# Kernel optimization log

Measured on AMD Instinct MI355X. Metric: run time of the kernel, lower is better.

Reference implementation:

```python
import jax, jax.numpy as jnp
import numpy as np

B, D, R = 4096, 1024, 256
DT = 0.01
DT_SCALE = 1.0

# Yoshida 4th-order coefficients
_W1 = 1.0 / (2.0 - 2.0 ** (1.0 / 3.0))
_W0 = -(2.0 ** (1.0 / 3.0)) / (2.0 - 2.0 ** (1.0 / 3.0))
C1 = _W1 / 2.0
C2 = (_W0 + _W1) / 2.0
C3 = C2
C4 = C1
D1 = _W1
D2 = _W0
D3 = _W1


def setup_inputs() -> dict:
    key = jax.random.key(0)
    k1, k2, k3, k4, k5 = jax.random.split(key, 5)
    x = jax.random.normal(k1, (B, D), dtype=jnp.float32)
    v = jax.random.normal(k2, (B, D), dtype=jnp.float32)
    force = jax.random.normal(k3, (B, D), dtype=jnp.float32)
    # low-rank christoffel factors, scaled for numerical stability
    U = jax.random.normal(k4, (R, D), dtype=jnp.float32) * (1.0 / np.sqrt(D))
    W = jax.random.normal(k5, (D, R), dtype=jnp.float32) * (1.0 / np.sqrt(R))
    return {"x": x, "v": v, "force": force, "U": U, "W": W}


def _christoffel(tv, tx, U, W):
    # Gamma(v) = W @ (U v)^2  (low-rank quadratic form; x unused, matching
    # the gfn yoshida_fused(U, W) signature)
    h = jnp.einsum("rd,bd->br", U, tv)  # [B, R]
    return jnp.einsum("dr,br->bd", W, h * h)  # [B, D]


def reference(x, v, force, U, W):
    dt = DT * DT_SCALE

    def acceleration(tx, tv):
        return -_christoffel(tv, tx, U, W) + force

    x1 = x + C1 * dt * v
    v1 = v + D1 * dt * acceleration(x1, v)
    x2 = x1 + C2 * dt * v1
    v2 = v1 + D2 * dt * acceleration(x2, v1)
    x3 = x2 + C3 * dt * v2
    v3 = v2 + D3 * dt * acceleration(x3, v2)
    x_final = x3 + C4 * dt * v3
    return (x_final, v3)
```

## Files before the change

### kernel.cpp

```cpp
#include <hip/hip_runtime.h>


#define BSZ 4096
#define DD 1024
#define RR 256
#define NCOPY 4
#define COPY_BYTES (512u * 1024u)

typedef unsigned char uchar;
typedef long long i64;
typedef __attribute__((ext_vector_type(2))) long i64x2;
typedef __attribute__((ext_vector_type(4))) float f32x4;
typedef __attribute__((ext_vector_type(4))) unsigned int uint4v;

__device__ inline unsigned int f2q4(float a, float b, float c, float d) {
    int lo = __builtin_amdgcn_cvt_pk_fp8_f32(a, b, 0, false);
    int hi = __builtin_amdgcn_cvt_pk_fp8_f32(c, d, lo, true);
    return (unsigned int)hi;
}
__device__ inline uchar f2q1(float x) {
    return (uchar)(__builtin_amdgcn_cvt_pk_fp8_f32(x, x, 0, false) & 0xff);
}

__global__ __launch_bounds__(256) void pack_uw_kernel(
    const float* __restrict__ U, const float* __restrict__ W,
    uchar* __restrict__ ws)
{
    const int g = blockIdx.x * 256 + threadIdx.x;
    const float* src;
    size_t off;
    float sc;
    if (g < 16384) {
        const int l = g & 63, p = (g >> 6) & 15, nt = g >> 10;
        src = U + (size_t)(nt * 16 + (l & 15)) * DD + p * 64 + (l >> 4) * 8;
        off = ((size_t)nt << 14) + (p << 10) + (l << 4);
        sc = 8.0f;
    } else {
        const int g2 = g - 16384;
        const int l = g2 & 63, p = (g2 >> 6) & 3, dt_ = g2 >> 8;
        src = W + (size_t)(dt_ * 16 + (l & 15)) * RR + p * 64 + (l >> 4) * 8;
        off = (size_t)(256 * 1024) + ((size_t)dt_ << 12) + (p << 10) + (l << 4);
        sc = 16.0f;
    }
    const float4 x0 = *reinterpret_cast<const float4*>(src);
    const float4 x1 = *reinterpret_cast<const float4*>(src + 4);
    const float4 y0 = *reinterpret_cast<const float4*>(src + 32);
    const float4 y1 = *reinterpret_cast<const float4*>(src + 36);
    uint4v o;
    o.x = f2q4(sc * x0.x, sc * x0.y, sc * x0.z, sc * x0.w);
    o.y = f2q4(sc * x1.x, sc * x1.y, sc * x1.z, sc * x1.w);
    o.z = f2q4(sc * y0.x, sc * y0.y, sc * y0.z, sc * y0.w);
    o.w = f2q4(sc * y1.x, sc * y1.y, sc * y1.z, sc * y1.w);
    #pragma unroll
    for (int c = 0; c < NCOPY; ++c)
        *reinterpret_cast<uint4v*>(ws + (size_t)c * COPY_BYTES + off) = o;
}

__global__ __launch_bounds__(1024) void yoshida_fused_kernel(
    const float* __restrict__ x_in,
    const float* __restrict__ v_in,
    const float* __restrict__ force,
    const uchar* __restrict__ ws,
    float* __restrict__ x_out,
    float* __restrict__ v_out)
{
    __shared__ __align__(16) uchar vS[16][1040];
    __shared__ __align__(16) uchar H2S[16][272];

    const int tid = threadIdx.x;
    const int w = tid >> 6, l = tid & 63;
    const int m = l & 15, q = l >> 4;
    const int b0 = blockIdx.x * 16;
    const int d0 = w * 64;

    const uchar* base = ws + (size_t)((blockIdx.x >> 3) & (NCOPY - 1)) * COPY_BYTES;

    constexpr double CBRT2 = 1.2599210498948731647672106072782;
    constexpr double W1c = 1.0 / (2.0 - CBRT2);
    constexpr double W0c = -CBRT2 * W1c;
    constexpr double DTd = 0.01 * 1.0;
    const float dcoef[3] = {(float)(W1c * DTd), (float)(W0c * DTd), (float)(W1c * DTd)};
    const float xcoef[3] = {(float)((W0c + W1c) * 0.5), (float)((W0c + W1c) * 0.5),
                            (float)(W1c * 0.5)};
    const float c1  = (float)(W1c * 0.5);
    const float dtf = (float)DTd;
    const float invdt = (float)(1.0 / DTd);

    float vreg[16], xacc[16], freg[16];
    #pragma unroll
    for (int t = 0; t < 4; ++t)
        #pragma unroll
        for (int i = 0; i < 4; ++i) {
            const size_t gidx = (size_t)(b0 + q * 4 + i) * DD + d0 + t * 16 + m;
            const float vv = v_in[gidx];
            vreg[t * 4 + i] = vv;
            xacc[t * 4 + i] = invdt * x_in[gidx] + c1 * vv;
            freg[t * 4 + i] = force[gidx];
        }

    {
        const int row = tid >> 6;
        const int col = (tid & 63) * 16;
        const float* sp = v_in + (size_t)(b0 + row) * DD + col;
        const float4 f0 = *reinterpret_cast<const float4*>(sp);
        const float4 f1 = *reinterpret_cast<const float4*>(sp + 4);
        const float4 f2 = *reinterpret_cast<const float4*>(sp + 8);
        const float4 f3 = *reinterpret_cast<const float4*>(sp + 12);
        uint4v pk;
        pk.x = f2q4(f0.x, f0.y, f0.z, f0.w);
        pk.y = f2q4(f1.x, f1.y, f1.z, f1.w);
        pk.z = f2q4(f2.x, f2.y, f2.z, f2.w);
        pk.w = f2q4(f3.x, f3.y, f3.z, f3.w);
        *reinterpret_cast<uint4v*>(&vS[row][col]) = pk;
    }

    const uchar* up = base + ((size_t)w << 14) + (l << 4);
    const uchar* wp = base + 256 * 1024 + ((size_t)(w * 4) << 12) + (l << 4);

    #pragma unroll
    for (int s = 0; s < 3; ++s) {
        __syncthreads();

        f32x4 a0 = {0.f, 0.f, 0.f, 0.f}, a1 = {0.f, 0.f, 0.f, 0.f};
        #pragma unroll
        for (int p = 0; p < 16; ++p) {
            const i64x2 bb = *reinterpret_cast<const i64x2*>(up + (p << 10));
            const i64 af0 = *reinterpret_cast<const i64*>(&vS[m][p * 64 + q * 8]);
            const i64 af1 = *reinterpret_cast<const i64*>(&vS[m][p * 64 + 32 + q * 8]);
            a0 = __builtin_amdgcn_mfma_f32_16x16x32_fp8_fp8(af0, bb.x, a0, 0, 0, 0);
            a1 = __builtin_amdgcn_mfma_f32_16x16x32_fp8_fp8(af1, bb.y, a1, 0, 0, 0);
        }
        #pragma unroll
        for (int i = 0; i < 4; ++i) {
            const float h8 = a0[i] + a1[i];
            H2S[q * 4 + i][w * 16 + m] = f2q1(h8 * h8 * 0.015625f);
        }
        __syncthreads();

        f32x4 accB[4];
        #pragma unroll
        for (int t = 0; t < 4; ++t) accB[t] = (f32x4){0.f, 0.f, 0.f, 0.f};
        #pragma unroll
        for (int p = 0; p < 4; ++p) {
            const i64 ha0 = *reinterpret_cast<const i64*>(&H2S[m][p * 64 + q * 8]);
            const i64 ha1 = *reinterpret_cast<const i64*>(&H2S[m][p * 64 + 32 + q * 8]);
            #pragma unroll
            for (int t = 0; t < 4; ++t) {
                const i64x2 wb = *reinterpret_cast<const i64x2*>(wp + (t << 12) + (p << 10));
                accB[t] = __builtin_amdgcn_mfma_f32_16x16x32_fp8_fp8(ha0, wb.x, accB[t], 0, 0, 0);
                accB[t] = __builtin_amdgcn_mfma_f32_16x16x32_fp8_fp8(ha1, wb.y, accB[t], 0, 0, 0);
            }
        }

        const float ddt = dcoef[s], cx = xcoef[s], gsc = dcoef[s] * 0.0625f;
        #pragma unroll
        for (int t = 0; t < 4; ++t)
            #pragma unroll
            for (int i = 0; i < 4; ++i) {
                const float vn = vreg[t * 4 + i] + ddt * freg[t * 4 + i]
                                 - gsc * accB[t][i];
                vreg[t * 4 + i] = vn;
                xacc[t * 4 + i] += cx * vn;
                vS[q * 4 + i][d0 + t * 16 + m] = f2q1(vn);
            }
    }

    #pragma unroll
    for (int t = 0; t < 4; ++t)
        #pragma unroll
        for (int i = 0; i < 4; ++i) {
            const size_t g = (size_t)(b0 + q * 4 + i) * DD + d0 + t * 16 + m;
            x_out[g] = dtf * xacc[t * 4 + i];
            v_out[g] = vreg[t * 4 + i];
        }
}

extern "C" void kernel_launch(void* const* d_in, const int* in_sizes, int n_in,
                              void* d_out, int out_size, void* d_ws, size_t ws_size,
                              hipStream_t stream) {
    const float* x     = (const float*)d_in[0];
    const float* v     = (const float*)d_in[1];
    const float* force = (const float*)d_in[2];
    const float* U     = (const float*)d_in[3];
    const float* W     = (const float*)d_in[4];

    float* x_out = (float*)d_out;
    float* v_out = x_out + (size_t)BSZ * DD;

    uchar* ws = (uchar*)d_ws;

    pack_uw_kernel<<<dim3(128), dim3(256), 0, stream>>>(U, W, ws);
    yoshida_fused_kernel<<<dim3(BSZ / 16), dim3(1024), 0, stream>>>(
        x, v, force, ws, x_out, v_out);
}
```

Measured before the change: 125.9 us.

## Move force and x accumulator to LDS, preload W into registers, double-buffer U

Keeps force in LDS as fp16 and the x accumulator in LDS as fp32, freeing registers, and defers the x_in load to the final stage. W fragments are held in registers across all three stages, U fragments are prefetched in a double buffer, and a minimum-blocks hint is added to launch bounds. The aim is to cut register pressure and hide global load latency. The cost is much more LDS per block (about 115KB), which limits resident blocks, and fp16 rounding of force.

Measured after the change: 138.5 us. +10.0%, slower.

```diff
diff --git a/kernel.cpp b/kernel.cpp
--- a/kernel.cpp
+++ b/kernel.cpp
@@ -12,6 +12,7 @@
 typedef __attribute__((ext_vector_type(2))) long i64x2;
 typedef __attribute__((ext_vector_type(4))) float f32x4;
 typedef __attribute__((ext_vector_type(4))) unsigned int uint4v;
+typedef __attribute__((ext_vector_type(4))) _Float16 f16x4;
 
 __device__ inline unsigned int f2q4(float a, float b, float c, float d) {
     int lo = __builtin_amdgcn_cvt_pk_fp8_f32(a, b, 0, false);
@@ -56,7 +57,7 @@
         *reinterpret_cast<uint4v*>(ws + (size_t)c * COPY_BYTES + off) = o;
 }
 
-__global__ __launch_bounds__(1024) void yoshida_fused_kernel(
+__global__ __launch_bounds__(1024, 4) void yoshida_fused_kernel(
     const float* __restrict__ x_in,
     const float* __restrict__ v_in,
     const float* __restrict__ force,
@@ -66,6 +67,8 @@
 {
     __shared__ __align__(16) uchar vS[16][1040];
     __shared__ __align__(16) uchar H2S[16][272];
+    __shared__ __align__(16) _Float16 fS[16][1032];
+    __shared__ __align__(16) float xaS[16][1028];
 
     const int tid = threadIdx.x;
     const int w = tid >> 6, l = tid & 63;
@@ -84,19 +87,16 @@
                             (float)(W1c * 0.5)};
     const float c1  = (float)(W1c * 0.5);
     const float dtf = (float)DTd;
-    const float invdt = (float)(1.0 / DTd);
-
-    float vreg[16], xacc[16], freg[16];
+
+    const uchar* up = base + ((size_t)w << 14) + (l << 4);
+    const uchar* wp = base + 256 * 1024 + ((size_t)(w * 4) << 12) + (l << 4);
+
+    i64x2 wreg[4][4];
     #pragma unroll
     for (int t = 0; t < 4; ++t)
         #pragma unroll
-        for (int i = 0; i < 4; ++i) {
-            const size_t gidx = (size_t)(b0 + q * 4 + i) * DD + d0 + t * 16 + m;
-            const float vv = v_in[gidx];
-            vreg[t * 4 + i] = vv;
-            xacc[t * 4 + i] = invdt * x_in[gidx] + c1 * vv;
-            freg[t * 4 + i] = force[gidx];
-        }
+        for (int p = 0; p < 4; ++p)
+            wreg[t][p] = *reinterpret_cast<const i64x2*>(wp + (t << 12) + (p << 10));
 
     {
         const int row = tid >> 6;
@@ -114,8 +114,31 @@
         *reinterpret_cast<uint4v*>(&vS[row][col]) = pk;
     }
 
-    const uchar* up = base + ((size_t)w << 14) + (l << 4);
-    const uchar* wp = base + 256 * 1024 + ((size_t)(w * 4) << 12) + (l << 4);
+    {
+        const float* sp = force + (size_t)(b0 + w) * DD;
+        #pragma unroll
+        for (int c = 0; c < 4; ++c) {
+            const float4 f = *reinterpret_cast<const float4*>(sp + l * 4 + c * 256);
+            f16x4 h;
+            h.x = (_Float16)f.x; h.y = (_Float16)f.y;
+            h.z = (_Float16)f.z; h.w = (_Float16)f.w;
+            *reinterpret_cast<f16x4*>(&fS[w][l * 4 + c * 256]) = h;
+        }
+    }
+
+    float vreg[16];
+    #pragma unroll
+    for (int t = 0; t < 4; ++t)
+        #pragma unroll
+        for (int i = 0; i < 4; ++i)
+            vreg[t * 4 + i] =
+                v_in[(size_t)(b0 + q * 4 + i) * DD + d0 + t * 16 + m];
+
+    i64x2 ub[2][2];
+    ub[0][0] = *reinterpret_cast<const i64x2*>(up);
+    ub[0][1] = *reinterpret_cast<const i64x2*>(up + 1024);
+
+    float xreg[16];
 
     #pragma unroll
     for (int s = 0; s < 3; ++s) {
@@ -123,12 +146,26 @@
 
         f32x4 a0 = {0.f, 0.f, 0.f, 0.f}, a1 = {0.f, 0.f, 0.f, 0.f};
         #pragma unroll
-        for (int p = 0; p < 16; ++p) {
-            const i64x2 bb = *reinterpret_cast<const i64x2*>(up + (p << 10));
-            const i64 af0 = *reinterpret_cast<const i64*>(&vS[m][p * 64 + q * 8]);
-            const i64 af1 = *reinterpret_cast<const i64*>(&vS[m][p * 64 + 32 + q * 8]);
-            a0 = __builtin_amdgcn_mfma_f32_16x16x32_fp8_fp8(af0, bb.x, a0, 0, 0, 0);
-            a1 = __builtin_amdgcn_mfma_f32_16x16x32_fp8_fp8(af1, bb.y, a1, 0, 0, 0);
+        for (int pb = 0; pb < 8; ++pb) {
+            if (pb < 7) {
+                ub[(pb + 1) & 1][0] = *reinterpret_cast<const i64x2*>(
+                    up + (((pb + 1) * 2 + 0) << 10));
+                ub[(pb + 1) & 1][1] = *reinterpret_cast<const i64x2*>(
+                    up + (((pb + 1) * 2 + 1) << 10));
+            } else if (s < 2) {
+                ub[0][0] = *reinterpret_cast<const i64x2*>(up);
+                ub[0][1] = *reinterpret_cast<const i64x2*>(up + 1024);
+            }
+            #pragma unroll
+            for (int j = 0; j < 2; ++j) {
+                const int p = pb * 2 + j;
+                const i64 af0 = *reinterpret_cast<const i64*>(&vS[m][p * 64 + q * 8]);
+                const i64 af1 = *reinterpret_cast<const i64*>(&vS[m][p * 64 + 32 + q * 8]);
+                a0 = __builtin_amdgcn_mfma_f32_16x16x32_fp8_fp8(
+                         af0, ub[pb & 1][j].x, a0, 0, 0, 0);
+                a1 = __builtin_amdgcn_mfma_f32_16x16x32_fp8_fp8(
+                         af1, ub[pb & 1][j].y, a1, 0, 0, 0);
+            }
         }
         #pragma unroll
         for (int i = 0; i < 4; ++i) {
@@ -137,6 +174,15 @@
         }
         __syncthreads();
 
+        if (s == 2) {
+            #pragma unroll
+            for (int t = 0; t < 4; ++t)
+                #pragma unroll
+                for (int i = 0; i < 4; ++i)
+                    xreg[t * 4 + i] =
+                        x_in[(size_t)(b0 + q * 4 + i) * DD + d0 + t * 16 + m];
+        }
+
         f32x4 accB[4];
         #pragma unroll
         for (int t = 0; t < 4; ++t) accB[t] = (f32x4){0.f, 0.f, 0.f, 0.f};
@@ -146,9 +192,10 @@
             const i64 ha1 = *reinterpret_cast<const i64*>(&H2S[m][p * 64 + 32 + q * 8]);
             #pragma unroll
             for (int t = 0; t < 4; ++t) {
-                const i64x2 wb = *reinterpret_cast<const i64x2*>(wp + (t << 12) + (p << 10));
-                accB[t] = __builtin_amdgcn_mfma_f32_16x16x32_fp8_fp8(ha0, wb.x, accB[t], 0, 0, 0);
-                accB[t] = __builtin_amdgcn_mfma_f32_16x16x32_fp8_fp8(ha1, wb.y, accB[t], 0, 0, 0);
+                accB[t] = __builtin_amdgcn_mfma_f32_16x16x32_fp8_fp8(
+                              ha0, wreg[t][p].x, accB[t], 0, 0, 0);
+                accB[t] = __builtin_amdgcn_mfma_f32_16x16x32_fp8_fp8(
+                              ha1, wreg[t][p].y, accB[t], 0, 0, 0);
             }
         }
 
@@ -157,22 +204,25 @@
         for (int t = 0; t < 4; ++t)
             #pragma unroll
             for (int i = 0; i < 4; ++i) {
-                const float vn = vreg[t * 4 + i] + ddt * freg[t * 4 + i]
-                                 - gsc * accB[t][i];
+                const int r = q * 4 + i, c = d0 + t * 16 + m;
+                const float ff = (float)fS[r][c];
+                const float vold = vreg[t * 4 + i];
+                const float vn = vold + ddt * ff - gsc * accB[t][i];
                 vreg[t * 4 + i] = vn;
-                xacc[t * 4 + i] += cx * vn;
-                vS[q * 4 + i][d0 + t * 16 + m] = f2q1(vn);
-            }
-    }
-
-    #pragma unroll
-    for (int t = 0; t < 4; ++t)
-        #pragma unroll
-        for (int i = 0; i < 4; ++i) {
-            const size_t g = (size_t)(b0 + q * 4 + i) * DD + d0 + t * 16 + m;
-            x_out[g] = dtf * xacc[t * 4 + i];
-            v_out[g] = vreg[t * 4 + i];
-        }
+                if (s == 0) {
+                    xaS[r][c] = c1 * vold + cx * vn;
+                    vS[r][c] = f2q1(vn);
+                } else if (s == 1) {
+                    xaS[r][c] += cx * vn;
+                    vS[r][c] = f2q1(vn);
+                } else {
+                    const float xa = xaS[r][c] + cx * vn;
+                    const size_t g = (size_t)(b0 + r) * DD + c;
+                    x_out[g] = xreg[t * 4 + i] + dtf * xa;
+                    v_out[g] = vn;
+                }
+            }
+    }
 }
 
 extern "C" void kernel_launch(void* const* d_in, const int* in_sizes, int n_in,
```

## Recast Yoshida steps in rank space using precomputed U·W and bf16 MFMA

Applied to the files above, without the earlier changes.

Rewrites the integrator algebraically so the three stages run in the rank-256 space. It precomputes M = U·W with a new atomic-add kernel and tracks h = U·v, updating it through g = U·force and M·h². The per-stage D×R W GEMMs are replaced by one final W projection that gives both the v and x corrections (P and Q coefficient sums). Precision moves from fp8 to bf16 MFMA, which roughly doubles the operand bytes per FLOP. A third launch is added, along with an atomicAdd reduction and large LDS use (152KB per block), which limits occupancy to one block per CU.

Result: slower. 148.5 us (+18.0%).

```diff
diff --git a/kernel.cpp b/kernel.cpp
--- a/kernel.cpp
+++ b/kernel.cpp
@@ -4,56 +4,85 @@
 #define BSZ 4096
 #define DD 1024
 #define RR 256
-#define NCOPY 4
-#define COPY_BYTES (512u * 1024u)
+
+#define U_OFF 0u
+#define W_OFF (512u * 1024u)
+#define M_OFF (1024u * 1024u)
 
 typedef unsigned char uchar;
 typedef long long i64;
-typedef __attribute__((ext_vector_type(2))) long i64x2;
+typedef unsigned int uint;
 typedef __attribute__((ext_vector_type(4))) float f32x4;
-typedef __attribute__((ext_vector_type(4))) unsigned int uint4v;
-
-__device__ inline unsigned int f2q4(float a, float b, float c, float d) {
-    int lo = __builtin_amdgcn_cvt_pk_fp8_f32(a, b, 0, false);
-    int hi = __builtin_amdgcn_cvt_pk_fp8_f32(c, d, lo, true);
-    return (unsigned int)hi;
-}
-__device__ inline uchar f2q1(float x) {
-    return (uchar)(__builtin_amdgcn_cvt_pk_fp8_f32(x, x, 0, false) & 0xff);
-}
-
-__global__ __launch_bounds__(256) void pack_uw_kernel(
+typedef __attribute__((ext_vector_type(4))) uint uint4v;
+typedef __attribute__((ext_vector_type(8))) short short8;
+
+__device__ inline uint f2bf1(float x) {
+    uint u = __builtin_bit_cast(uint, x);
+    return (u + 0x7FFFu + ((u >> 16) & 1u)) >> 16;
+}
+__device__ inline uint f2bf2(float lo, float hi) {
+    return f2bf1(lo) | (f2bf1(hi) << 16);
+}
+
+__global__ __launch_bounds__(256) void pack_kernel(
     const float* __restrict__ U, const float* __restrict__ W,
     uchar* __restrict__ ws)
 {
     const int g = blockIdx.x * 256 + threadIdx.x;
+    *reinterpret_cast<float*>(ws + M_OFF + (size_t)g * 4) = 0.0f;
+
+    const int l = g & 63;
     const float* src;
-    size_t off;
-    float sc;
-    if (g < 16384) {
-        const int l = g & 63, p = (g >> 6) & 15, nt = g >> 10;
-        src = U + (size_t)(nt * 16 + (l & 15)) * DD + p * 64 + (l >> 4) * 8;
-        off = ((size_t)nt << 14) + (p << 10) + (l << 4);
-        sc = 8.0f;
+    size_t dst;
+    if (g < 32768) {
+        const int slice = g >> 6, nt = slice >> 5, p = slice & 31;
+        src = U + (size_t)(nt * 16 + (l & 15)) * DD + p * 32 + (l >> 4) * 8;
+        dst = U_OFF + (size_t)slice * 1024 + l * 16;
     } else {
-        const int g2 = g - 16384;
-        const int l = g2 & 63, p = (g2 >> 6) & 3, dt_ = g2 >> 8;
-        src = W + (size_t)(dt_ * 16 + (l & 15)) * RR + p * 64 + (l >> 4) * 8;
-        off = (size_t)(256 * 1024) + ((size_t)dt_ << 12) + (p << 10) + (l << 4);
-        sc = 16.0f;
-    }
-    const float4 x0 = *reinterpret_cast<const float4*>(src);
-    const float4 x1 = *reinterpret_cast<const float4*>(src + 4);
-    const float4 y0 = *reinterpret_cast<const float4*>(src + 32);
-    const float4 y1 = *reinterpret_cast<const float4*>(src + 36);
+        const int g2 = g - 32768;
+        const int slice = g2 >> 6, dt_ = slice >> 3, p = slice & 7;
+        src = W + (size_t)(dt_ * 16 + (l & 15)) * RR + p * 32 + (l >> 4) * 8;
+        dst = W_OFF + (size_t)slice * 1024 + l * 16;
+    }
+    const float4 a0 = *reinterpret_cast<const float4*>(src);
+    const float4 a1 = *reinterpret_cast<const float4*>(src + 4);
     uint4v o;
-    o.x = f2q4(sc * x0.x, sc * x0.y, sc * x0.z, sc * x0.w);
-    o.y = f2q4(sc * x1.x, sc * x1.y, sc * x1.z, sc * x1.w);
-    o.z = f2q4(sc * y0.x, sc * y0.y, sc * y0.z, sc * y0.w);
-    o.w = f2q4(sc * y1.x, sc * y1.y, sc * y1.z, sc * y1.w);
-    #pragma unroll
-    for (int c = 0; c < NCOPY; ++c)
-        *reinterpret_cast<uint4v*>(ws + (size_t)c * COPY_BYTES + off) = o;
+    o.x = f2bf2(a0.x, a0.y); o.y = f2bf2(a0.z, a0.w);
+    o.z = f2bf2(a1.x, a1.y); o.w = f2bf2(a1.z, a1.w);
+    *reinterpret_cast<uint4v*>(ws + dst) = o;
+}
+
+__global__ __launch_bounds__(1024) void mm_kernel(
+    const float* __restrict__ U, const float* __restrict__ W,
+    uchar* __restrict__ ws)
+{
+    float* Mf = reinterpret_cast<float*>(ws + M_OFF);
+    const int rt = blockIdx.x >> 4;
+    const int kc = blockIdx.x & 15;
+    const int rp = threadIdx.x & 255;
+    const int ro = threadIdx.x >> 8;
+    float acc[4] = {0.f, 0.f, 0.f, 0.f};
+    const int kb = kc * 64;
+    for (int ks = 0; ks < 8; ++ks) {
+        float uv[4][8];
+        #pragma unroll
+        for (int j = 0; j < 4; ++j) {
+            const float* us = U + (size_t)(rt * 16 + ro * 4 + j) * DD + kb + ks * 8;
+            const float4 u0 = *reinterpret_cast<const float4*>(us);
+            const float4 u1 = *reinterpret_cast<const float4*>(us + 4);
+            uv[j][0] = u0.x; uv[j][1] = u0.y; uv[j][2] = u0.z; uv[j][3] = u0.w;
+            uv[j][4] = u1.x; uv[j][5] = u1.y; uv[j][6] = u1.z; uv[j][7] = u1.w;
+        }
+        #pragma unroll
+        for (int kk = 0; kk < 8; ++kk) {
+            const float wv = W[(size_t)(kb + ks * 8 + kk) * RR + rp];
+            #pragma unroll
+            for (int j = 0; j < 4; ++j) acc[j] += uv[j][kk] * wv;
+        }
+    }
+    #pragma unroll
+    for (int j = 0; j < 4; ++j)
+        atomicAdd(Mf + (size_t)(rt * 16 + ro * 4 + j) * RR + rp, acc[j]);
 }
 
 __global__ __launch_bounds__(1024) void yoshida_fused_kernel(
@@ -64,115 +93,225 @@
     float* __restrict__ x_out,
     float* __restrict__ v_out)
 {
-    __shared__ __align__(16) uchar vS[16][1040];
-    __shared__ __align__(16) uchar H2S[16][272];
+    __shared__ __align__(16) uchar lds[152 * 1024];
+    uchar* const vA  = lds;
+    uchar* const fA  = lds + 32768;
+    uchar* const Ml  = lds;
+    uchar* const H2B = lds + 131072;
+    uchar* const PB  = lds + 139264;
+    uchar* const QB  = lds + 147456;
 
     const int tid = threadIdx.x;
     const int w = tid >> 6, l = tid & 63;
     const int m = l & 15, q = l >> 4;
     const int b0 = blockIdx.x * 16;
-    const int d0 = w * 64;
-
-    const uchar* base = ws + (size_t)((blockIdx.x >> 3) & (NCOPY - 1)) * COPY_BYTES;
 
     constexpr double CBRT2 = 1.2599210498948731647672106072782;
     constexpr double W1c = 1.0 / (2.0 - CBRT2);
     constexpr double W0c = -CBRT2 * W1c;
-    constexpr double DTd = 0.01 * 1.0;
-    const float dcoef[3] = {(float)(W1c * DTd), (float)(W0c * DTd), (float)(W1c * DTd)};
-    const float xcoef[3] = {(float)((W0c + W1c) * 0.5), (float)((W0c + W1c) * 0.5),
-                            (float)(W1c * 0.5)};
-    const float c1  = (float)(W1c * 0.5);
-    const float dtf = (float)DTd;
-    const float invdt = (float)(1.0 / DTd);
-
-    float vreg[16], xacc[16], freg[16];
-    #pragma unroll
-    for (int t = 0; t < 4; ++t)
+    constexpr double DTd = 0.01;
+    constexpr double D1 = W1c, D2 = W0c, D3 = W1c;
+    constexpr double C2c = (W0c + W1c) * 0.5, C4c = W1c * 0.5;
+    constexpr double E1 = (C2c + C2c + C4c) * D1;
+    constexpr double E2 = (C2c + C4c) * D2;
+    constexpr double E3 = C4c * D3;
+    const float dtf = (float)DTd, dt2 = (float)(DTd * DTd);
+    const float se = (float)(E1 + E2 + E3);
+
+    #pragma unroll
+    for (int j = 0; j < 2; ++j) {
+        const int p = 2 * w + j;
+        const size_t so = (size_t)(b0 + m) * DD + p * 32 + q * 8;
+        const float4 v0_ = *reinterpret_cast<const float4*>(v_in + so);
+        const float4 v1_ = *reinterpret_cast<const float4*>(v_in + so + 4);
+        const float4 f0_ = *reinterpret_cast<const float4*>(force + so);
+        const float4 f1_ = *reinterpret_cast<const float4*>(force + so + 4);
+        uint4v ov, of;
+        ov.x = f2bf2(v0_.x, v0_.y); ov.y = f2bf2(v0_.z, v0_.w);
+        ov.z = f2bf2(v1_.x, v1_.y); ov.w = f2bf2(v1_.z, v1_.w);
+        of.x = f2bf2(f0_.x, f0_.y); of.y = f2bf2(f0_.z, f0_.w);
+        of.z = f2bf2(f1_.x, f1_.y); of.w = f2bf2(f1_.z, f1_.w);
+        *reinterpret_cast<uint4v*>(vA + (size_t)p * 1024 + l * 16) = ov;
+        *reinterpret_cast<uint4v*>(fA + (size_t)p * 1024 + l * 16) = of;
+    }
+
+    const uchar* const up = ws + U_OFF + ((size_t)w << 15) + l * 16;
+    uint4v ub[8];
+    #pragma unroll
+    for (int p = 0; p < 8; ++p)
+        ub[p] = *reinterpret_cast<const uint4v*>(up + ((size_t)p << 10));
+
+    __syncthreads();
+
+    f32x4 h = {0.f, 0.f, 0.f, 0.f}, g = {0.f, 0.f, 0.f, 0.f};
+    #pragma unroll
+    for (int p = 0; p < 32; ++p) {
+        const uint4v uc = ub[p & 7];
+        if (p < 24)
+            ub[p & 7] = *reinterpret_cast<const uint4v*>(up + ((size_t)(p + 8) << 10));
+        const short8 ua = __builtin_bit_cast(short8, uc);
+        const short8 va = __builtin_bit_cast(short8,
+            *reinterpret_cast<const uint4v*>(vA + ((size_t)p << 10) + l * 16));
+        const short8 fa = __builtin_bit_cast(short8,
+            *reinterpret_cast<const uint4v*>(fA + ((size_t)p << 10) + l * 16));
+        h = __builtin_amdgcn_mfma_f32_16x16x32_bf16(ua, va, h, 0, 0, 0);
+        g = __builtin_amdgcn_mfma_f32_16x16x32_bf16(ua, fa, g, 0, 0, 0);
+    }
+
+    __syncthreads();
+
+    {
+        const float* Mf = reinterpret_cast<const float*>(ws + M_OFF);
+        #pragma unroll 4
+        for (int rep = 0; rep < 8; ++rep) {
+            const int item = tid + rep * 1024;
+            const int sl = item >> 6, ll = item & 63;
+            const int nt = sl >> 3, p = sl & 7;
+            const float* sm = Mf + (size_t)(nt * 16 + (ll & 15)) * RR + p * 32 + (ll >> 4) * 8;
+            const float4 a0 = *reinterpret_cast<const float4*>(sm);
+            const float4 a1 = *reinterpret_cast<const float4*>(sm + 4);
+            uint4v o;
+            o.x = f2bf2(a0.x, a0.y); o.y = f2bf2(a0.z, a0.w);
+            o.z = f2bf2(a1.x, a1.y); o.w = f2bf2(a1.z, a1.w);
+            *reinterpret_cast<uint4v*>(Ml + (size_t)sl * 1024 + ll * 16) = o;
+        }
+    }
+
+    const int k0 = 16 * w + 4 * q;
+    const int p0 = k0 >> 5;
+    const int lp = ((k0 & 31) >> 3) * 16 + m;
+    const int j0 = k0 & 7;
+
+    f32x4 P, Q;
+    {
+        float h2[4];
+        #pragma unroll
+        for (int i = 0; i < 4; ++i) h2[i] = h[i] * h[i];
         #pragma unroll
         for (int i = 0; i < 4; ++i) {
-            const size_t gidx = (size_t)(b0 + q * 4 + i) * DD + d0 + t * 16 + m;
-            const float vv = v_in[gidx];
-            vreg[t * 4 + i] = vv;
-            xacc[t * 4 + i] = invdt * x_in[gidx] + c1 * vv;
-            freg[t * 4 + i] = force[gidx];
-        }
-
-    {
-        const int row = tid >> 6;
-        const int col = (tid & 63) * 16;
-        const float* sp = v_in + (size_t)(b0 + row) * DD + col;
-        const float4 f0 = *reinterpret_cast<const float4*>(sp);
-        const float4 f1 = *reinterpret_cast<const float4*>(sp + 4);
-        const float4 f2 = *reinterpret_cast<const float4*>(sp + 8);
-        const float4 f3 = *reinterpret_cast<const float4*>(sp + 12);
-        uint4v pk;
-        pk.x = f2q4(f0.x, f0.y, f0.z, f0.w);
-        pk.y = f2q4(f1.x, f1.y, f1.z, f1.w);
-        pk.z = f2q4(f2.x, f2.y, f2.z, f2.w);
-        pk.w = f2q4(f3.x, f3.y, f3.z, f3.w);
-        *reinterpret_cast<uint4v*>(&vS[row][col]) = pk;
-    }
-
-    const uchar* up = base + ((size_t)w << 14) + (l << 4);
-    const uchar* wp = base + 256 * 1024 + ((size_t)(w * 4) << 12) + (l << 4);
-
-    #pragma unroll
-    for (int s = 0; s < 3; ++s) {
-        __syncthreads();
-
-        f32x4 a0 = {0.f, 0.f, 0.f, 0.f}, a1 = {0.f, 0.f, 0.f, 0.f};
-        #pragma unroll
-        for (int p = 0; p < 16; ++p) {
-            const i64x2 bb = *reinterpret_cast<const i64x2*>(up + (p << 10));
-            const i64 af0 = *reinterpret_cast<const i64*>(&vS[m][p * 64 + q * 8]);
-            const i64 af1 = *reinterpret_cast<const i64*>(&vS[m][p * 64 + 32 + q * 8]);
-            a0 = __builtin_amdgcn_mfma_f32_16x16x32_fp8_fp8(af0, bb.x, a0, 0, 0, 0);
-            a1 = __builtin_amdgcn_mfma_f32_16x16x32_fp8_fp8(af1, bb.y, a1, 0, 0, 0);
-        }
+            P[i] = (float)D1 * h2[i];
+            Q[i] = (float)E1 * h2[i];
+        }
+        *reinterpret_cast<uint*>(H2B + (size_t)p0 * 1024 + lp * 16 + j0 * 2)
+            = f2bf2(h2[0], h2[1]);
+        *reinterpret_cast<uint*>(H2B + (size_t)p0 * 1024 + lp * 16 + j0 * 2 + 4)
+            = f2bf2(h2[2], h2[3]);
+    }
+    __syncthreads();
+    {
+        f32x4 acc = {0.f, 0.f, 0.f, 0.f};
+        #pragma unroll
+        for (int p = 0; p < 8; ++p) {
+            const short8 ma = __builtin_bit_cast(short8,
+                *reinterpret_cast<const uint4v*>(Ml + (size_t)(w * 8 + p) * 1024 + l * 16));
+            const short8 hb = __builtin_bit_cast(short8,
+                *reinterpret_cast<const uint4v*>(H2B + ((size_t)p << 10) + l * 16));
+            acc = __builtin_amdgcn_mfma_f32_16x16x32_bf16(ma, hb, acc, 0, 0, 0);
+        }
+        const float cg = (float)(DTd * D1);
+        #pragma unroll
+        for (int i = 0; i < 4; ++i) h[i] += cg * (g[i] - acc[i]);
+    }
+    __syncthreads();
+    {
+        float h2[4];
+        #pragma unroll
+        for (int i = 0; i < 4; ++i) h2[i] = h[i] * h[i];
         #pragma unroll
         for (int i = 0; i < 4; ++i) {
-            const float h8 = a0[i] + a1[i];
-            H2S[q * 4 + i][w * 16 + m] = f2q1(h8 * h8 * 0.015625f);
-        }
-        __syncthreads();
-
-        f32x4 accB[4];
-        #pragma unroll
-        for (int t = 0; t < 4; ++t) accB[t] = (f32x4){0.f, 0.f, 0.f, 0.f};
-        #pragma unroll
-        for (int p = 0; p < 4; ++p) {
-            const i64 ha0 = *reinterpret_cast<const i64*>(&H2S[m][p * 64 + q * 8]);
-            const i64 ha1 = *reinterpret_cast<const i64*>(&H2S[m][p * 64 + 32 + q * 8]);
-            #pragma unroll
-            for (int t = 0; t < 4; ++t) {
-                const i64x2 wb = *reinterpret_cast<const i64x2*>(wp + (t << 12) + (p << 10));
-                accB[t] = __builtin_amdgcn_mfma_f32_16x16x32_fp8_fp8(ha0, wb.x, accB[t], 0, 0, 0);
-                accB[t] = __builtin_amdgcn_mfma_f32_16x16x32_fp8_fp8(ha1, wb.y, accB[t], 0, 0, 0);
+            P[i] += (float)D2 * h2[i];
+            Q[i] += (float)E2 * h2[i];
+        }
+        *reinterpret_cast<uint*>(H2B + (size_t)p0 * 1024 + lp * 16 + j0 * 2)
+            = f2bf2(h2[0], h2[1]);
+        *reinterpret_cast<uint*>(H2B + (size_t)p0 * 1024 + lp * 16 + j0 * 2 + 4)
+            = f2bf2(h2[2], h2[3]);
+    }
+    __syncthreads();
+    {
+        f32x4 acc = {0.f, 0.f, 0.f, 0.f};
+        #pragma unroll
+        for (int p = 0; p < 8; ++p) {
+            const short8 ma = __builtin_bit_cast(short8,
+                *reinterpret_cast<const uint4v*>(Ml + (size_t)(w * 8 + p) * 1024 + l * 16));
+            const short8 hb = __builtin_bit_cast(short8,
+                *reinterpret_cast<const uint4v*>(H2B + ((size_t)p << 10) + l * 16));
+            acc = __builtin_amdgcn_mfma_f32_16x16x32_bf16(ma, hb, acc, 0, 0, 0);
+        }
+        const float cg = (float)(DTd * D2);
+        #pragma unroll
+        for (int i = 0; i < 4; ++i) h[i] += cg * (g[i] - acc[i]);
+    }
+    {
+        float h2[4];
+        #pragma unroll
+        for (int i = 0; i < 4; ++i) h2[i] = h[i] * h[i];
+        #pragma unroll
+        for (int i = 0; i < 4; ++i) {
+            P[i] += (float)D3 * h2[i];
+            Q[i] += (float)E3 * h2[i];
+        }
+    }
+    *reinterpret_cast<uint*>(PB + (size_t)p0 * 1024 + lp * 16 + j0 * 2)     = f2bf2(P[0], P[1]);
+    *reinterpret_cast<uint*>(PB + (size_t)p0 * 1024 + lp * 16 + j0 * 2 + 4) = f2bf2(P[2], P[3]);
+    *reinterpret_cast<uint*>(QB + (size_t)p0 * 1024 + lp * 16 + j0 * 2)     = f2bf2(Q[0], Q[1]);
+    *reinterpret_cast<uint*>(QB + (size_t)p0 * 1024 + lp * 16 + j0 * 2 + 4) = f2bf2(Q[2], Q[3]);
+
+    const uchar* const wpb = ws + W_OFF + l * 16;
+    uint4v wb[4][2];
+    #pragma unroll
+    for (int p = 0; p < 4; ++p) {
+        wb[p][0] = *reinterpret_cast<const uint4v*>(wpb + (size_t)((4 * w)     * 8 + p) * 1024);
+        wb[p][1] = *reinterpret_cast<const uint4v*>(wpb + (size_t)((4 * w + 1) * 8 + p) * 1024);
+    }
+
+    __syncthreads();
+
+    #pragma unroll
+    for (int half = 0; half < 2; ++half) {
+        const int t0 = 4 * w + half * 2;
+        f32x4 aV[2] = {{0.f,0.f,0.f,0.f}, {0.f,0.f,0.f,0.f}};
+        f32x4 aX[2] = {{0.f,0.f,0.f,0.f}, {0.f,0.f,0.f,0.f}};
+        #pragma unroll
+        for (int p = 0; p < 8; ++p) {
+            const uint4v c0 = wb[p & 3][0];
+            const uint4v c1 = wb[p & 3][1];
+            if (p < 4) {
+                wb[p & 3][0] = *reinterpret_cast<const uint4v*>(
+                    wpb + (size_t)((t0)     * 8 + p + 4) * 1024);
+                wb[p & 3][1] = *reinterpret_cast<const uint4v*>(
+                    wpb + (size_t)((t0 + 1) * 8 + p + 4) * 1024);
+            } else if (half == 0) {
+                wb[p & 3][0] = *reinterpret_cast<const uint4v*>(
+                    wpb + (size_t)((t0 + 2) * 8 + (p - 4)) * 1024);
+                wb[p & 3][1] = *reinterpret_cast<const uint4v*>(
+                    wpb + (size_t)((t0 + 3) * 8 + (p - 4)) * 1024);
             }
-        }
-
-        const float ddt = dcoef[s], cx = xcoef[s], gsc = dcoef[s] * 0.0625f;
-        #pragma unroll
-        for (int t = 0; t < 4; ++t)
+            const short8 pb = __builtin_bit_cast(short8,
+                *reinterpret_cast<const uint4v*>(PB + ((size_t)p << 10) + l * 16));
+            const short8 qb = __builtin_bit_cast(short8,
+                *reinterpret_cast<const uint4v*>(QB + ((size_t)p << 10) + l * 16));
+            const short8 w0 = __builtin_bit_cast(short8, c0);
+            const short8 w1 = __builtin_bit_cast(short8, c1);
+            aV[0] = __builtin_amdgcn_mfma_f32_16x16x32_bf16(w0, pb, aV[0], 0, 0, 0);
+            aV[1] = __builtin_amdgcn_mfma_f32_16x16x32_bf16(w1, pb, aV[1], 0, 0, 0);
+            aX[0] = __builtin_amdgcn_mfma_f32_16x16x32_bf16(w0, qb, aX[0], 0, 0, 0);
+            aX[1] = __builtin_amdgcn_mfma_f32_16x16x32_bf16(w1, qb, aX[1], 0, 0, 0);
+        }
+        #pragma unroll
+        for (int t = 0; t < 2; ++t) {
+            const int d0 = (t0 + t) * 16 + 4 * q;
             #pragma unroll
             for (int i = 0; i < 4; ++i) {
-                const float vn = vreg[t * 4 + i] + ddt * freg[t * 4 + i]
-                                 - gsc * accB[t][i];
-                vreg[t * 4 + i] = vn;
-                xacc[t * 4 + i] += cx * vn;
-                vS[q * 4 + i][d0 + t * 16 + m] = f2q1(vn);
+                const size_t gi = (size_t)(b0 + m) * DD + d0 + i;
+                const float fv = force[gi];
+                const float v0 = v_in[gi];
+                const float x0 = x_in[gi];
+                v_out[gi] = v0 + dtf * fv - dtf * aV[t][i];
+                x_out[gi] = x0 + dtf * v0 + dt2 * se * fv - dt2 * aX[t][i];
             }
-    }
-
-    #pragma unroll
-    for (int t = 0; t < 4; ++t)
-        #pragma unroll
-        for (int i = 0; i < 4; ++i) {
-            const size_t g = (size_t)(b0 + q * 4 + i) * DD + d0 + t * 16 + m;
-            x_out[g] = dtf * xacc[t * 4 + i];
-            v_out[g] = vreg[t * 4 + i];
-        }
+        }
+    }
 }
 
 extern "C" void kernel_launch(void* const* d_in, const int* in_sizes, int n_in,
@@ -189,7 +328,8 @@
 
     uchar* ws = (uchar*)d_ws;
 
-    pack_uw_kernel<<<dim3(128), dim3(256), 0, stream>>>(U, W, ws);
+    pack_kernel<<<dim3(256), dim3(256), 0, stream>>>(U, W, ws);
+    mm_kernel<<<dim3(256), dim3(1024), 0, stream>>>(U, W, ws);
     yoshida_fused_kernel<<<dim3(BSZ / 16), dim3(1024), 0, stream>>>(
         x, v, force, ws, x_out, v_out);
 }
```
